# Performance work log

Measured on AMD Instinct MI355X. Metric: run time of the kernel, lower is better.

The kernel has to match this reference:

```python
import jax, jax.numpy as jnp
import numpy as np

B, K, N = 32768, 8, 64
TN = 3 * N


def _P():
    # 9x9 vec-transpose permutation (matches the hand-built P in the torch module)
    P = np.zeros((9, 9), dtype=np.float32)
    rows = [0, 1, 2, 3, 4, 5, 6, 7, 8]
    cols = [0, 3, 6, 1, 4, 7, 2, 5, 8]
    P[rows, cols] = 1.0
    return jnp.asarray(P)


def _precompute(b, w, lam):
    # b: (K,3,N), w: (1,N,1), lam: scalar
    wsum = jnp.sum(w)
    b_w = (b @ w)[..., 0] / wsum                       # (K,3)
    sw = jnp.sqrt(w).reshape(1, 1, N)                  # (1,1,N)
    bar_b = sw * (b - b_w[:, :, None])                 # (K,3,N)
    bar_B = bar_b.transpose(0, 2, 1).reshape(K, TN).T  # (3N,K)
    bar_H = 2.0 * (bar_B.T @ bar_B + lam * jnp.eye(K, dtype=b.dtype))
    Hinv = jnp.linalg.inv(bar_H)
    Htemp = Hinv @ jnp.ones((K, 1), dtype=b.dtype)     # (K,1)
    s = jnp.sum(Htemp)
    G = Hinv - (Htemp @ Htemp.T) / s                   # (K,K)
    g = Htemp / s                                      # (K,1)
    M = jnp.concatenate([
        2.0 * bar_B @ (G @ bar_B.T) - jnp.eye(TN, dtype=b.dtype),  # (3N,3N)
        2.0 * jnp.sqrt(lam) * (G @ bar_B.T),                        # (K,3N)
    ], axis=0)                                         # (3N+K,3N)
    h = jnp.concatenate([bar_B @ g, jnp.sqrt(lam) * g], axis=0)  # (3N+K,1)
    return bar_B, G, g, M, h, b_w, wsum


def setup_inputs() -> dict:
    key = jax.random.key(0)
    k1, k2 = jax.random.split(key)
    y = jax.random.normal(k1, (B, 3, N), dtype=jnp.float32)
    b = jax.random.normal(k2, (K, 3, N), dtype=jnp.float32)
    w = jnp.ones((1, N, 1), dtype=jnp.float32)
    lam = jnp.ones((1,), dtype=jnp.float32)
    return {"y": y, "b": b, "w": w, "lam": lam}


def reference(y, b, w, lam):
    lam = jnp.squeeze(lam)
    Pm = _P()
    bar_B, G, g, M, h, b_w, wsum = _precompute(b, w, lam)

    # weighted centroid + centered/weighted keypoints
    y_w = (y @ w) / wsum                               # (B,3,1)
    sw = jnp.sqrt(w).reshape(1, 1, N)
    bar_y = sw * (y - y_w)                             # (B,3,N)

    # Batched Q build. kron(Y^T, I3) contraction done implicitly:
    # (M @ kron(Y^T,I3))[a, 3m+j] = sum_n M[a,3n+j] * Y[m,n]
    M_r = M.reshape(TN + K, N, 3)                      # (A,N,3)
    E = jnp.einsum('anj,bmn->bamj', M_r, bar_y).reshape(B, TN + K, 9) @ Pm  # tempE: (B,A,9)
    q_top = jnp.einsum('a,bae->be', h[:, 0], E)        # Q[0,1:]: (B,9)
    Q00 = jnp.sum(h * h)
    Q_low = jnp.einsum('bae,baf->bef', E, E)           # Q[1:,1:]: (B,9,9)

    Q = jnp.zeros((B, 10, 10), dtype=y.dtype)
    Q = Q.at[:, 0, 0].set(Q00)
    Q = Q.at[:, 0, 1:].set(q_top)
    Q = Q.at[:, 1:, 0].set(q_top)
    Q = Q.at[:, 1:, 1:].set(Q_low)

    # Tight SDP relaxation solution: X* = v v^T with v the eigenvector of Q
    # at the smallest eigenvalue; the original then takes top eigvec of X,
    # which recovers the same v.
    ev, evec = jnp.linalg.eigh(Q)
    vec = evec[:, :, 0]                                # smallest-eigenvalue eigvec, (B,10)
    vec = vec / vec[:, :1]
    R = vec[:, 1:].reshape(B, 3, 3).transpose(0, 2, 1)  # (B,3,3)

    # shape coefficients: c = 2 * G bar_B^T kron(I_N, R^T) vec(bar_y^T) + g
    A = G @ bar_B.T                                    # (K,3N)
    Bv = jnp.einsum('bji,bjn->bni', R, bar_y).reshape(B, TN, 1)
    c = 2.0 * (A @ Bv) + g                             # (B,K,1)

    # translation
    t = y_w - R @ (b_w.T @ c)                          # (B,3,1)
    return R, t, c
```

## Files before the change

### kernel.cpp

```cpp
#include <hip/hip_runtime.h>
#include <math.h>

static constexpr int Bn = 32768;

#define WS_COEF  0
#define WS_G     1792
#define WS_g     1856
#define WS_BW    1864
#define WS_Q00   1888
#define WS_WSUM  1889
#define WS_CB    2048

__host__ __device__ constexpr int tidx(int i, int j) { return i*10 - i*(i+1)/2 + j; }
__host__ __device__ constexpr int tmm(int i, int j)  { return (i<j) ? tidx(i,j) : tidx(j,i); }
__host__ __device__ constexpr int lidx(int i, int j) { return i*(i+1)/2 + j; }

__global__ void k_pre(const float* __restrict__ bb, const float* __restrict__ w,
                      const float* __restrict__ lam, float* __restrict__ ws)
{
  __shared__ float s_w[64], s_sw[64], s_bw[24], s_barb[64][24];
  __shared__ float s_BtB[64];
  __shared__ float s_M[8][16];
  __shared__ float s_u[8], s_g[8], s_red[64], s_wsum, s_s;
  const int t = threadIdx.x;
  const int i8 = t >> 3, j8 = t & 7;
  const float lv = lam[0];

  s_w[t]  = w[t];
  s_sw[t] = sqrtf(fmaxf(s_w[t], 0.0f));
  __syncthreads();
  if (t == 0) { float a = 0; for (int n = 0; n < 64; n++) a += s_w[n]; s_wsum = a; }
  __syncthreads();
  const float wsum = s_wsum;
  if (t < 24) {
    float a = 0;
    for (int n = 0; n < 64; n++) a += bb[t*64 + n] * s_w[n];
    s_bw[t] = a / wsum;
  }
  __syncthreads();
  for (int km = 0; km < 24; ++km)
    s_barb[t][km] = s_sw[t] * (bb[km*64 + t] - s_bw[km]);
  __syncthreads();
  {
    float a = 0;
    for (int n = 0; n < 64; n++)
      for (int j = 0; j < 3; j++)
        a += s_barb[n][i8*3 + j] * s_barb[n][j8*3 + j];
    s_BtB[t] = a;
  }
  __syncthreads();
  s_M[i8][j8]     = 2.0f * (s_BtB[t] + ((i8 == j8) ? lv : 0.0f));
  s_M[i8][8 + j8] = (i8 == j8) ? 1.0f : 0.0f;
#pragma unroll
  for (int k = 0; k < 8; k++) {
    __syncthreads();
    const float fk  = s_M[i8][k];
    const float piv = 1.0f / s_M[k][k];
    __syncthreads();
    if (i8 == k) { s_M[k][j8] *= piv; s_M[k][8 + j8] *= piv; }
    __syncthreads();
    if (i8 != k) {
      s_M[i8][j8]     -= fk * s_M[k][j8];
      s_M[i8][8 + j8] -= fk * s_M[k][8 + j8];
    }
  }
  __syncthreads();
  if (t < 8) {
    float a = 0;
#pragma unroll
    for (int j = 0; j < 8; j++) a += s_M[t][8 + j];
    s_u[t] = a;
  }
  __syncthreads();
  if (t == 0) {
    float s = 0;
#pragma unroll
    for (int j = 0; j < 8; j++) s += s_u[j];
    s_s = s;
  }
  __syncthreads();
  const float s = s_s;
  if (t < 8) s_g[t] = s_u[t] / s;
  const float Gel = s_M[i8][8 + j8] - s_u[i8] * s_u[j8] / s;
  ws[WS_G + t] = Gel;
  __syncthreads();
  s_red[t] = s_g[i8] * (s_BtB[t] + ((i8 == j8) ? lv : 0.0f)) * s_g[j8];
  __syncthreads();
  if (t == 0) {
    float a = 0;
    for (int n = 0; n < 64; n++) a += s_red[n];
    ws[WS_Q00]  = a;
    ws[WS_WSUM] = wsum;
  }
  if (t < 8)  ws[WS_g + t]  = s_g[t];
  if (t < 24) ws[WS_BW + t] = s_bw[t];
  {
    float* c = ws + WS_COEF + t*28;
    c[0] = s_w[t];
    float qc[3] = {0, 0, 0};
#pragma unroll
    for (int km = 0; km < 24; km++) {
      float cb = s_sw[t] * s_barb[t][km];
      c[4 + km] = cb;
      qc[km % 3] += s_g[km / 3] * cb;
    }
    c[1] = qc[0]; c[2] = qc[1]; c[3] = qc[2];
  }
  {
#pragma unroll
    for (int sub = 0; sub < 4; sub++) {
      float* p = ws + WS_CB + sub*520 + t*8;
      p[0] = s_w[t];
#pragma unroll
      for (int kk = 0; kk < 6; kk++)
        p[1 + kk] = s_sw[t] * s_barb[t][sub*6 + kk];
      p[7] = 0.0f;
    }
  }
}

__global__ __launch_bounds__(256, 2) void k_main(const float* __restrict__ y,
                                                 const float* __restrict__ ws,
                                                 float* __restrict__ out)
{
  __shared__ float s_cb[4*520];
  __shared__ float s_G[64], s_g8[8], s_bw[24];
  __shared__ float s_F[72][66];
  __shared__ float s_Q[55][66];
  const int t   = threadIdx.x;
  const int lb  = t >> 2;
  const int sub = t & 3;
  const int b   = blockIdx.x * 64 + lb;

  for (int i = t; i < 4*520; i += 256) s_cb[i] = ws[WS_CB + i];
  if (t < 64) s_G[t]  = ws[WS_G + t];
  if (t < 8)  s_g8[t] = ws[WS_g + t];
  if (t >= 8 && t < 32) s_bw[t - 8] = ws[WS_BW + (t - 8)];
  const float q00v = ws[WS_Q00];
  const float wsum = ws[WS_WSUM];
  __syncthreads();

  const float* yb = y + (size_t)b * 192;
  float F6[6][3];
  float gw[6];
  float ywa[3] = {0, 0, 0};
#pragma unroll
  for (int i = 0; i < 6; i++) { F6[i][0] = 0; F6[i][1] = 0; F6[i][2] = 0; gw[i] = 0; }

  const float4* cbp = reinterpret_cast<const float4*>(s_cb + sub*520);
  for (int n4 = 0; n4 < 16; n4++) {
    float4 v0 = reinterpret_cast<const float4*>(yb)[n4];
    float4 v1 = reinterpret_cast<const float4*>(yb + 64)[n4];
    float4 v2 = reinterpret_cast<const float4*>(yb + 128)[n4];
    float a0[4] = {v0.x, v0.y, v0.z, v0.w};
    float a1[4] = {v1.x, v1.y, v1.z, v1.w};
    float a2[4] = {v2.x, v2.y, v2.z, v2.w};
#pragma unroll
    for (int l = 0; l < 4; l++) {
      const int n = 4*n4 + l;
      float4 va = cbp[n*2], vb = cbp[n*2 + 1];
      const float cb[6] = {va.y, va.z, va.w, vb.x, vb.y, vb.z};
      float ym0 = a0[l], ym1 = a1[l], ym2 = a2[l];
      float wn  = va.x;
      float wy0 = wn*ym0, wy1 = wn*ym1, wy2 = wn*ym2;
      ywa[0] += wy0; ywa[1] += wy1; ywa[2] += wy2;
      gw[0] += wy0*ym0; gw[1] += wy0*ym1; gw[2] += wy0*ym2;
      gw[3] += wy1*ym1; gw[4] += wy1*ym2; gw[5] += wy2*ym2;
#pragma unroll
      for (int kk = 0; kk < 6; kk++) {
        F6[kk][0] += cb[kk]*ym0; F6[kk][1] += cb[kk]*ym1; F6[kk][2] += cb[kk]*ym2;
      }
    }
  }
  const float iws = 1.0f / wsum;
  float yw[3] = {ywa[0]*iws, ywa[1]*iws, ywa[2]*iws};
  float Gram[6];
  Gram[0] = gw[0] - ywa[0]*ywa[0]*iws;
  Gram[1] = gw[1] - ywa[0]*ywa[1]*iws;
  Gram[2] = gw[2] - ywa[0]*ywa[2]*iws;
  Gram[3] = gw[3] - ywa[1]*ywa[1]*iws;
  Gram[4] = gw[4] - ywa[1]*ywa[2]*iws;
  Gram[5] = gw[5] - ywa[2]*ywa[2]*iws;

  const int kj0 = sub * 6;
#pragma unroll
  for (int kk = 0; kk < 6; kk++)
#pragma unroll
    for (int m = 0; m < 3; m++)
      s_F[(kj0 + kk)*3 + m][lb] = F6[kk][m];
  if (sub == 0) s_Q[0][lb] = q00v;
  {
    const float g0 = s_g8[sub*2], g1 = s_g8[sub*2 + 1];
#pragma unroll
    for (int e = 0; e < 9; e++) {
      const int j = e / 3, m = e % 3;
      float p = g0 * F6[j][m] + g1 * F6[3 + j][m];
      p += __shfl_xor(p, 1);
      p += __shfl_xor(p, 2);
      if ((e & 3) == sub) s_Q[tidx(0, 1 + e)][lb] = -p;
    }
  }
  __syncthreads();

  float FGr[2][9];
#pragma unroll
  for (int kk = 0; kk < 2; kk++) {
    const int k2 = sub*2 + kk;
    float gcol[8];
#pragma unroll
    for (int k = 0; k < 8; k++) gcol[k] = s_G[k*8 + k2];
#pragma unroll
    for (int e = 0; e < 9; e++) {
      const int j = e / 3, m = e % 3;
      float a = 0;
#pragma unroll
      for (int k = 0; k < 8; k++) a += gcol[k] * s_F[(k*3 + j)*3 + m][lb];
      FGr[kk][e] = a;
    }
  }
#pragma unroll
  for (int e = 0; e < 9; e++)
#pragma unroll
    for (int f = e; f < 9; f++) {
      const int j = e/3, m = e%3, j2 = f/3, m2 = f%3;
      float p = FGr[0][e] * F6[j2][m2] + FGr[1][e] * F6[3 + j2][m2];
      p += __shfl_xor(p, 1);
      p += __shfl_xor(p, 2);
      if ((tidx(1 + e, 1 + f) & 3) == sub) {
        const float gterm = (j == j2) ? Gram[(m <= m2) ? (m*3 - m*(m+1)/2 + m2) : (m2*3 - m2*(m2+1)/2 + m)] : 0.0f;
        s_Q[tidx(1 + e, 1 + f)][lb] = -2.0f*p + gterm;
      }
    }
  __syncthreads();

  float Mm[55];
#pragma unroll
  for (int i = 0; i < 10; i++)
#pragma unroll
    for (int j = 0; j <= i; j++)
      Mm[lidx(i,j)] = s_Q[tidx(j,i)][lb];

  float ad[10], b2[9];
#pragma unroll
  for (int j = 0; j < 8; j++) {
    float s2 = 0;
#pragma unroll
    for (int i = j + 1; i < 10; i++) s2 += Mm[lidx(i,j)] * Mm[lidx(i,j)];
    const float x0 = Mm[lidx(j+1,j)];
    const float anorm = __builtin_amdgcn_sqrtf(s2);
    const float alpha = (x0 > 0.0f) ? -anorm : anorm;
    const float uu = s2 - alpha * x0;
    const float beta = (uu > 1e-35f) ? __builtin_amdgcn_rcpf(uu) : 0.0f;
    float u[10], p[10];
    u[j+1] = x0 - alpha;
#pragma unroll
    for (int i = j + 2; i < 10; i++) u[i] = Mm[lidx(i,j)];
#pragma unroll
    for (int i = j + 1; i < 10; i++) {
      float acc = 0;
#pragma unroll
      for (int k = j + 1; k < 10; k++) acc += Mm[(i >= k) ? lidx(i,k) : lidx(k,i)] * u[k];
      p[i] = beta * acc;
    }
    float K = 0;
#pragma unroll
    for (int i = j + 1; i < 10; i++) K += u[i] * p[i];
    K *= 0.5f * beta;
#pragma unroll
    for (int i = j + 1; i < 10; i++) p[i] -= K * u[i];
#pragma unroll
    for (int i = j + 1; i < 10; i++)
#pragma unroll
      for (int k = j + 1; k <= i; k++)
        Mm[lidx(i,k)] -= u[i]*p[k] + p[i]*u[k];
    ad[j] = Mm[lidx(j,j)];
    b2[j] = s2;
  }
  ad[8] = Mm[lidx(8,8)];
  ad[9] = Mm[lidx(9,9)];
  b2[8] = Mm[lidx(9,8)] * Mm[lidx(9,8)];

  float b2max = b2[0];
#pragma unroll
  for (int i = 1; i < 9; i++) b2max = fmaxf(b2max, b2[i]);
  const float pm = 1e-20f * b2max + 1e-30f;

  float lo = 0.0f, hi = s_Q[0][lb];
#pragma unroll
  for (int j = 1; j < 10; j++) hi = fminf(hi, s_Q[tidx(j,j)][lb]);

  const int base = (t & 63) & ~3;
  const float subf = (sub == 0) ? 2.0f : (float)sub;
  for (int round = 0; round < 11; ++round) {
    const float quart = 0.25f * (hi - lo);
    const float mid = lo + quart * subf;
    int neg = 0;
    float d = ad[0] - mid;
    neg += (d < 0.0f) ? 1 : 0;
#pragma unroll
    for (int i = 1; i < 10; i++) {
      d = (fabsf(d) < pm) ? -pm : d;
      d = ad[i] - mid - b2[i-1] * __builtin_amdgcn_rcpf(d);
      neg += (d < 0.0f) ? 1 : 0;
    }
    const int n1 = __shfl(neg, base | 1);
    const int n2 = __shfl(neg, base | 2);
    const int n3 = __shfl(neg, base | 3);
    const float m1 = lo + quart, m2v = lo + 2.0f*quart, m3 = lo + 3.0f*quart;
    const float nlo = (n3 == 0) ? m3 : (n2 == 0) ? m2v : (n1 == 0) ? m1 : lo;
    const float nhi = (n1 > 0) ? m1 : (n2 > 0) ? m2v : (n3 > 0) ? m3 : hi;
    lo = nlo; hi = nhi;
  }

  float M[55], id[10];
#pragma unroll
  for (int i = 0; i < 10; i++)
#pragma unroll
    for (int j = 0; j <= i; j++)
      M[lidx(i,j)] = s_Q[tidx(j,i)][lb];
  float tr = 0.0f;
#pragma unroll
  for (int i = 0; i < 10; i++) tr += M[lidx(i,i)];
  const float delta = 1e-5f * fabsf(tr) + 1e-30f;
  const float sigma = lo - delta;
#pragma unroll
  for (int i = 0; i < 10; i++) M[lidx(i,i)] -= sigma;

#pragma unroll
  for (int j = 0; j < 10; j++) {
    float d = M[lidx(j,j)];
#pragma unroll
    for (int t2 = 0; t2 < j; t2++) d -= M[lidx(j,t2)] * M[lidx(j,t2)];
    d = fmaxf(d, 1e-30f);
    float is = __builtin_amdgcn_rsqf(d);
    id[j] = is;
#pragma unroll
    for (int i = j + 1; i < 10; i++) {
      float a = M[lidx(i,j)];
#pragma unroll
      for (int t2 = 0; t2 < j; t2++) a -= M[lidx(i,t2)] * M[lidx(j,t2)];
      M[lidx(i,j)] = a * is;
    }
  }

  float x[10];
#pragma unroll
  for (int i = 0; i < 10; i++) x[i] = 1.0f;
#pragma unroll
  for (int it = 0; it < 3; ++it) {
#pragma unroll
    for (int i = 0; i < 10; i++) {
      float a = x[i];
#pragma unroll
      for (int j = 0; j < i; j++) a -= M[lidx(i,j)] * x[j];
      x[i] = a * id[i];
    }
#pragma unroll
    for (int i = 9; i >= 0; i--) {
      float a = x[i];
#pragma unroll
      for (int j = i + 1; j < 10; j++) a -= M[lidx(j,i)] * x[j];
      x[i] = a * id[i];
    }
    float s2 = 0;
#pragma unroll
    for (int i = 0; i < 10; i++) s2 += x[i]*x[i];
    float sc = __builtin_amdgcn_rsqf(s2 + 1e-38f);
#pragma unroll
    for (int i = 0; i < 10; i++) x[i] *= sc;
  }

  const float inv0 = __builtin_amdgcn_rcpf(x[0]);
  float R[3][3];
#pragma unroll
  for (int r = 0; r < 3; r++)
#pragma unroll
    for (int cc = 0; cc < 3; cc++)
      R[r][cc] = x[1 + 3*cc + r] * inv0;

  float cv[2];
#pragma unroll
  for (int kk = 0; kk < 2; kk++) {
    const int k = sub*2 + kk;
    float a = 0;
#pragma unroll
    for (int e = 0; e < 9; e++) a += x[1 + e] * FGr[kk][e];
    cv[kk] = 2.0f * inv0 * a + s_g8[k];
    out[(size_t)12*Bn + (size_t)b*8 + k] = cv[kk];
  }
  float um0 = s_bw[(sub*2)*3 + 0]*cv[0] + s_bw[(sub*2 + 1)*3 + 0]*cv[1];
  float um1 = s_bw[(sub*2)*3 + 1]*cv[0] + s_bw[(sub*2 + 1)*3 + 1]*cv[1];
  float um2 = s_bw[(sub*2)*3 + 2]*cv[0] + s_bw[(sub*2 + 1)*3 + 2]*cv[1];
  um0 += __shfl_xor(um0, 1); um0 += __shfl_xor(um0, 2);
  um1 += __shfl_xor(um1, 1); um1 += __shfl_xor(um1, 2);
  um2 += __shfl_xor(um2, 1); um2 += __shfl_xor(um2, 2);

#pragma unroll
  for (int r = 0; r < 3; r++)
#pragma unroll
    for (int cc = 0; cc < 3; cc++)
      if (((r*3 + cc) & 3) == sub)
        out[(size_t)b*9 + r*3 + cc] = R[r][cc];
  if (sub == 0) {
#pragma unroll
    for (int r = 0; r < 3; r++)
      out[(size_t)9*Bn + (size_t)b*3 + r] = yw[r] - (R[r][0]*um0 + R[r][1]*um1 + R[r][2]*um2);
  }
}

extern "C" void kernel_launch(void* const* d_in, const int* in_sizes, int n_in,
                              void* d_out, int out_size, void* d_ws, size_t ws_size,
                              hipStream_t stream) {
  const float* y   = (const float*)d_in[0];
  const float* bb  = (const float*)d_in[1];
  const float* w   = (const float*)d_in[2];
  const float* lam = (const float*)d_in[3];
  float* ws  = (float*)d_ws;
  float* out = (float*)d_out;
  k_pre <<<1,      64, 0, stream>>>(bb, w, lam, ws);
  k_main<<<Bn/64, 256, 0, stream>>>(y, ws, out);
}
```

Baseline: 42.90 us.

## Split each batch item across eight lanes and use 9-way bisection

Each batch element is now handled by eight threads instead of four, so each lane owns one shape coefficient k. Block size grows to 512 threads and the precomputed coefficient table is repacked to four floats per point per lane. The eigenvalue bisection now tests eight points per round (splitting the interval into nine parts) and runs fewer rounds. The aim is more parallelism and shorter per-thread dependency chains, at the cost of redundant reads of y (now duplicated across eight lanes), an extra shuffle level in every reduction, and duplicated eigensolve work.

```diff
diff --git a/kernel.cpp b/kernel.cpp
--- a/kernel.cpp
+++ b/kernel.cpp
@@ -3,16 +3,14 @@
 
 static constexpr int Bn = 32768;
 
-#define WS_COEF  0
 #define WS_G     1792
 #define WS_g     1856
 #define WS_BW    1864
 #define WS_Q00   1888
 #define WS_WSUM  1889
-#define WS_CB    2048
+#define WS_CB8   2048
 
 __host__ __device__ constexpr int tidx(int i, int j) { return i*10 - i*(i+1)/2 + j; }
-__host__ __device__ constexpr int tmm(int i, int j)  { return (i<j) ? tidx(i,j) : tidx(j,i); }
 __host__ __device__ constexpr int lidx(int i, int j) { return i*(i+1)/2 + j; }
 
 __global__ void k_pre(const float* __restrict__ bb, const float* __restrict__ w,
@@ -95,44 +93,31 @@
   if (t < 8)  ws[WS_g + t]  = s_g[t];
   if (t < 24) ws[WS_BW + t] = s_bw[t];
   {
-    float* c = ws + WS_COEF + t*28;
-    c[0] = s_w[t];
-    float qc[3] = {0, 0, 0};
-#pragma unroll
-    for (int km = 0; km < 24; km++) {
-      float cb = s_sw[t] * s_barb[t][km];
-      c[4 + km] = cb;
-      qc[km % 3] += s_g[km / 3] * cb;
-    }
-    c[1] = qc[0]; c[2] = qc[1]; c[3] = qc[2];
-  }
-  {
-#pragma unroll
-    for (int sub = 0; sub < 4; sub++) {
-      float* p = ws + WS_CB + sub*520 + t*8;
+#pragma unroll
+    for (int sub = 0; sub < 8; sub++) {
+      float* p = ws + WS_CB8 + sub*260 + t*4;
       p[0] = s_w[t];
 #pragma unroll
-      for (int kk = 0; kk < 6; kk++)
-        p[1 + kk] = s_sw[t] * s_barb[t][sub*6 + kk];
-      p[7] = 0.0f;
+      for (int kk = 0; kk < 3; kk++)
+        p[1 + kk] = s_sw[t] * s_barb[t][sub*3 + kk];
     }
   }
 }
 
-__global__ __launch_bounds__(256, 2) void k_main(const float* __restrict__ y,
+__global__ __launch_bounds__(512, 4) void k_main(const float* __restrict__ y,
                                                  const float* __restrict__ ws,
                                                  float* __restrict__ out)
 {
-  __shared__ float s_cb[4*520];
+  __shared__ float s_cb[8*260];
   __shared__ float s_G[64], s_g8[8], s_bw[24];
   __shared__ float s_F[72][66];
   __shared__ float s_Q[55][66];
   const int t   = threadIdx.x;
-  const int lb  = t >> 2;
-  const int sub = t & 3;
+  const int lb  = t >> 3;
+  const int sub = t & 7;
   const int b   = blockIdx.x * 64 + lb;
 
-  for (int i = t; i < 4*520; i += 256) s_cb[i] = ws[WS_CB + i];
+  for (int i = t; i < 8*260; i += 512) s_cb[i] = ws[WS_CB8 + i];
   if (t < 64) s_G[t]  = ws[WS_G + t];
   if (t < 8)  s_g8[t] = ws[WS_g + t];
   if (t >= 8 && t < 32) s_bw[t - 8] = ws[WS_BW + (t - 8)];
@@ -141,13 +126,15 @@
   __syncthreads();
 
   const float* yb = y + (size_t)b * 192;
-  float F6[6][3];
+  float F3[3][3];
   float gw[6];
   float ywa[3] = {0, 0, 0};
 #pragma unroll
-  for (int i = 0; i < 6; i++) { F6[i][0] = 0; F6[i][1] = 0; F6[i][2] = 0; gw[i] = 0; }
-
-  const float4* cbp = reinterpret_cast<const float4*>(s_cb + sub*520);
+  for (int i = 0; i < 3; i++) { F3[i][0] = 0; F3[i][1] = 0; F3[i][2] = 0; }
+#pragma unroll
+  for (int i = 0; i < 6; i++) gw[i] = 0;
+
+  const float4* cbp = reinterpret_cast<const float4*>(s_cb + sub*260);
   for (int n4 = 0; n4 < 16; n4++) {
     float4 v0 = reinterpret_cast<const float4*>(yb)[n4];
     float4 v1 = reinterpret_cast<const float4*>(yb + 64)[n4];
@@ -158,8 +145,8 @@
 #pragma unroll
     for (int l = 0; l < 4; l++) {
       const int n = 4*n4 + l;
-      float4 va = cbp[n*2], vb = cbp[n*2 + 1];
-      const float cb[6] = {va.y, va.z, va.w, vb.x, vb.y, vb.z};
+      float4 va = cbp[n];
+      const float cb3[3] = {va.y, va.z, va.w};
       float ym0 = a0[l], ym1 = a1[l], ym2 = a2[l];
       float wn  = va.x;
       float wy0 = wn*ym0, wy1 = wn*ym1, wy2 = wn*ym2;
@@ -167,8 +154,8 @@
       gw[0] += wy0*ym0; gw[1] += wy0*ym1; gw[2] += wy0*ym2;
       gw[3] += wy1*ym1; gw[4] += wy1*ym2; gw[5] += wy2*ym2;
 #pragma unroll
-      for (int kk = 0; kk < 6; kk++) {
-        F6[kk][0] += cb[kk]*ym0; F6[kk][1] += cb[kk]*ym1; F6[kk][2] += cb[kk]*ym2;
+      for (int kk = 0; kk < 3; kk++) {
+        F3[kk][0] += cb3[kk]*ym0; F3[kk][1] += cb3[kk]*ym1; F3[kk][2] += cb3[kk]*ym2;
       }
     }
   }
@@ -182,40 +169,38 @@
   Gram[4] = gw[4] - ywa[1]*ywa[2]*iws;
   Gram[5] = gw[5] - ywa[2]*ywa[2]*iws;
 
-  const int kj0 = sub * 6;
-#pragma unroll
-  for (int kk = 0; kk < 6; kk++)
+#pragma unroll
+  for (int kk = 0; kk < 3; kk++)
 #pragma unroll
     for (int m = 0; m < 3; m++)
-      s_F[(kj0 + kk)*3 + m][lb] = F6[kk][m];
+      s_F[(sub*3 + kk)*3 + m][lb] = F3[kk][m];
   if (sub == 0) s_Q[0][lb] = q00v;
   {
-    const float g0 = s_g8[sub*2], g1 = s_g8[sub*2 + 1];
+    const float g0 = s_g8[sub];
 #pragma unroll
     for (int e = 0; e < 9; e++) {
       const int j = e / 3, m = e % 3;
-      float p = g0 * F6[j][m] + g1 * F6[3 + j][m];
+      float p = g0 * F3[j][m];
       p += __shfl_xor(p, 1);
       p += __shfl_xor(p, 2);
-      if ((e & 3) == sub) s_Q[tidx(0, 1 + e)][lb] = -p;
-    }
-  }
-  __syncthreads();
-
-  float FGr[2][9];
-#pragma unroll
-  for (int kk = 0; kk < 2; kk++) {
-    const int k2 = sub*2 + kk;
+      p += __shfl_xor(p, 4);
+      if ((e & 7) == sub) s_Q[tidx(0, 1 + e)][lb] = -p;
+    }
+  }
+  __syncthreads();
+
+  float FGr[9];
+  {
     float gcol[8];
 #pragma unroll
-    for (int k = 0; k < 8; k++) gcol[k] = s_G[k*8 + k2];
+    for (int k = 0; k < 8; k++) gcol[k] = s_G[k*8 + sub];
 #pragma unroll
     for (int e = 0; e < 9; e++) {
       const int j = e / 3, m = e % 3;
       float a = 0;
 #pragma unroll
       for (int k = 0; k < 8; k++) a += gcol[k] * s_F[(k*3 + j)*3 + m][lb];
-      FGr[kk][e] = a;
+      FGr[e] = a;
     }
   }
 #pragma unroll
@@ -223,10 +208,11 @@
 #pragma unroll
     for (int f = e; f < 9; f++) {
       const int j = e/3, m = e%3, j2 = f/3, m2 = f%3;
-      float p = FGr[0][e] * F6[j2][m2] + FGr[1][e] * F6[3 + j2][m2];
+      float p = FGr[e] * F3[j2][m2];
       p += __shfl_xor(p, 1);
       p += __shfl_xor(p, 2);
-      if ((tidx(1 + e, 1 + f) & 3) == sub) {
+      p += __shfl_xor(p, 4);
+      if ((tidx(1 + e, 1 + f) & 7) == sub) {
         const float gterm = (j == j2) ? Gram[(m <= m2) ? (m*3 - m*(m+1)/2 + m2) : (m2*3 - m2*(m2+1)/2 + m)] : 0.0f;
         s_Q[tidx(1 + e, 1 + f)][lb] = -2.0f*p + gterm;
       }
@@ -289,11 +275,11 @@
 #pragma unroll
   for (int j = 1; j < 10; j++) hi = fminf(hi, s_Q[tidx(j,j)][lb]);
 
-  const int base = (t & 63) & ~3;
-  const float subf = (sub == 0) ? 2.0f : (float)sub;
-  for (int round = 0; round < 11; ++round) {
-    const float quart = 0.25f * (hi - lo);
-    const float mid = lo + quart * subf;
+  const int base = (t & 63) & ~7;
+  const float ninth = 1.0f / 9.0f;
+  for (int round = 0; round < 7; ++round) {
+    const float h9 = ninth * (hi - lo);
+    const float mid = lo + (float)(sub + 1) * h9;
     int neg = 0;
     float d = ad[0] - mid;
     neg += (d < 0.0f) ? 1 : 0;
@@ -303,12 +289,17 @@
       d = ad[i] - mid - b2[i-1] * __builtin_amdgcn_rcpf(d);
       neg += (d < 0.0f) ? 1 : 0;
     }
-    const int n1 = __shfl(neg, base | 1);
-    const int n2 = __shfl(neg, base | 2);
-    const int n3 = __shfl(neg, base | 3);
-    const float m1 = lo + quart, m2v = lo + 2.0f*quart, m3 = lo + 3.0f*quart;
-    const float nlo = (n3 == 0) ? m3 : (n2 == 0) ? m2v : (n1 == 0) ? m1 : lo;
-    const float nhi = (n1 > 0) ? m1 : (n2 > 0) ? m2v : (n3 > 0) ? m3 : hi;
+    int j = 0;
+    j = (__shfl(neg, base + 0) == 0) ? 1 : j;
+    j = (__shfl(neg, base + 1) == 0) ? 2 : j;
+    j = (__shfl(neg, base + 2) == 0) ? 3 : j;
+    j = (__shfl(neg, base + 3) == 0) ? 4 : j;
+    j = (__shfl(neg, base + 4) == 0) ? 5 : j;
+    j = (__shfl(neg, base + 5) == 0) ? 6 : j;
+    j = (__shfl(neg, base + 6) == 0) ? 7 : j;
+    j = (__shfl(neg, base + 7) == 0) ? 8 : j;
+    const float nlo = lo + (float)j * h9;
+    const float nhi = lo + (float)(j + 1) * h9;
     lo = nlo; hi = nhi;
   }
 
@@ -378,30 +369,28 @@
     for (int cc = 0; cc < 3; cc++)
       R[r][cc] = x[1 + 3*cc + r] * inv0;
 
-  float cv[2];
-#pragma unroll
-  for (int kk = 0; kk < 2; kk++) {
-    const int k = sub*2 + kk;
+  float cv;
+  {
     float a = 0;
 #pragma unroll
-    for (int e = 0; e < 9; e++) a += x[1 + e] * FGr[kk][e];
-    cv[kk] = 2.0f * inv0 * a + s_g8[k];
-    out[(size_t)12*Bn + (size_t)b*8 + k] = cv[kk];
-  }
-  float um0 = s_bw[(sub*2)*3 + 0]*cv[0] + s_bw[(sub*2 + 1)*3 + 0]*cv[1];
-  float um1 = s_bw[(sub*2)*3 + 1]*cv[0] + s_bw[(sub*2 + 1)*3 + 1]*cv[1];
-  float um2 = s_bw[(sub*2)*3 + 2]*cv[0] + s_bw[(sub*2 + 1)*3 + 2]*cv[1];
-  um0 += __shfl_xor(um0, 1); um0 += __shfl_xor(um0, 2);
-  um1 += __shfl_xor(um1, 1); um1 += __shfl_xor(um1, 2);
-  um2 += __shfl_xor(um2, 1); um2 += __shfl_xor(um2, 2);
+    for (int e = 0; e < 9; e++) a += x[1 + e] * FGr[e];
+    cv = 2.0f * inv0 * a + s_g8[sub];
+    out[(size_t)12*Bn + (size_t)b*8 + sub] = cv;
+  }
+  float um0 = s_bw[sub*3 + 0] * cv;
+  float um1 = s_bw[sub*3 + 1] * cv;
+  float um2 = s_bw[sub*3 + 2] * cv;
+  um0 += __shfl_xor(um0, 1); um0 += __shfl_xor(um0, 2); um0 += __shfl_xor(um0, 4);
+  um1 += __shfl_xor(um1, 1); um1 += __shfl_xor(um1, 2); um1 += __shfl_xor(um1, 4);
+  um2 += __shfl_xor(um2, 1); um2 += __shfl_xor(um2, 2); um2 += __shfl_xor(um2, 4);
 
 #pragma unroll
   for (int r = 0; r < 3; r++)
 #pragma unroll
     for (int cc = 0; cc < 3; cc++)
-      if (((r*3 + cc) & 3) == sub)
+      if (((r*3 + cc) & 7) == sub)
         out[(size_t)b*9 + r*3 + cc] = R[r][cc];
-  if (sub == 0) {
+  if (sub == 1) {
 #pragma unroll
     for (int r = 0; r < 3; r++)
       out[(size_t)9*Bn + (size_t)b*3 + r] = yw[r] - (R[r][0]*um0 + R[r][1]*um1 + R[r][2]*um2);
@@ -418,5 +407,5 @@
   float* ws  = (float*)d_ws;
   float* out = (float*)d_out;
   k_pre <<<1,      64, 0, stream>>>(bb, w, lam, ws);
-  k_main<<<Bn/64, 256, 0, stream>>>(y, ws, out);
+  k_main<<<Bn/64, 512, 0, stream>>>(y, ws, out);
 }
```

Measured after the change: 65.16 us. 1.52x slower.

## Split keypoint loop across lanes and reduce full F via shuffles

Applied to the files above, without the earlier changes.

Changes the work split among the four threads per batch element. Before, each thread handled six of the 24 coefficient columns over all 64 points. Now each thread handles 16 points for all 24 columns, and the partial sums of F, Gram and centroid are combined with xor shuffles. This removes the shared s_F staging buffer and one block barrier, and the coefficient table becomes a single 64x32 layout. In exchange each thread holds 72 F accumulators and runs 81 shuffle reductions, which raises register pressure under launch_bounds(256,2). A leftover no-op loop computing ci is also added.

```diff
diff --git a/kernel.cpp b/kernel.cpp
--- a/kernel.cpp
+++ b/kernel.cpp
@@ -3,16 +3,14 @@
 
 static constexpr int Bn = 32768;
 
-#define WS_COEF  0
 #define WS_G     1792
 #define WS_g     1856
 #define WS_BW    1864
 #define WS_Q00   1888
 #define WS_WSUM  1889
-#define WS_CB    2048
+#define WS_CB32  2048
 
 __host__ __device__ constexpr int tidx(int i, int j) { return i*10 - i*(i+1)/2 + j; }
-__host__ __device__ constexpr int tmm(int i, int j)  { return (i<j) ? tidx(i,j) : tidx(j,i); }
 __host__ __device__ constexpr int lidx(int i, int j) { return i*(i+1)/2 + j; }
 
 __global__ void k_pre(const float* __restrict__ bb, const float* __restrict__ w,
@@ -95,27 +93,13 @@
   if (t < 8)  ws[WS_g + t]  = s_g[t];
   if (t < 24) ws[WS_BW + t] = s_bw[t];
   {
-    float* c = ws + WS_COEF + t*28;
-    c[0] = s_w[t];
-    float qc[3] = {0, 0, 0};
-#pragma unroll
-    for (int km = 0; km < 24; km++) {
-      float cb = s_sw[t] * s_barb[t][km];
-      c[4 + km] = cb;
-      qc[km % 3] += s_g[km / 3] * cb;
-    }
-    c[1] = qc[0]; c[2] = qc[1]; c[3] = qc[2];
-  }
-  {
-#pragma unroll
-    for (int sub = 0; sub < 4; sub++) {
-      float* p = ws + WS_CB + sub*520 + t*8;
-      p[0] = s_w[t];
-#pragma unroll
-      for (int kk = 0; kk < 6; kk++)
-        p[1 + kk] = s_sw[t] * s_barb[t][sub*6 + kk];
-      p[7] = 0.0f;
-    }
+    float* p = ws + WS_CB32 + t*32;
+    p[0] = s_w[t]; p[1] = 0; p[2] = 0; p[3] = 0;
+#pragma unroll
+    for (int km = 0; km < 24; km++)
+      p[4 + km] = s_sw[t] * s_barb[t][km];
+#pragma unroll
+    for (int i = 28; i < 32; i++) p[i] = 0;
   }
 }
 
@@ -123,16 +107,15 @@
                                                  const float* __restrict__ ws,
                                                  float* __restrict__ out)
 {
-  __shared__ float s_cb[4*520];
+  __shared__ float s_cb[64*32];
   __shared__ float s_G[64], s_g8[8], s_bw[24];
-  __shared__ float s_F[72][66];
   __shared__ float s_Q[55][66];
   const int t   = threadIdx.x;
   const int lb  = t >> 2;
   const int sub = t & 3;
   const int b   = blockIdx.x * 64 + lb;
 
-  for (int i = t; i < 4*520; i += 256) s_cb[i] = ws[WS_CB + i];
+  for (int i = t; i < 64*32; i += 256) s_cb[i] = ws[WS_CB32 + i];
   if (t < 64) s_G[t]  = ws[WS_G + t];
   if (t < 8)  s_g8[t] = ws[WS_g + t];
   if (t >= 8 && t < 32) s_bw[t - 8] = ws[WS_BW + (t - 8)];
@@ -141,14 +124,17 @@
   __syncthreads();
 
   const float* yb = y + (size_t)b * 192;
-  float F6[6][3];
+  float F[24][3];
   float gw[6];
   float ywa[3] = {0, 0, 0};
 #pragma unroll
-  for (int i = 0; i < 6; i++) { F6[i][0] = 0; F6[i][1] = 0; F6[i][2] = 0; gw[i] = 0; }
-
-  const float4* cbp = reinterpret_cast<const float4*>(s_cb + sub*520);
-  for (int n4 = 0; n4 < 16; n4++) {
+  for (int i = 0; i < 24; i++) { F[i][0] = 0; F[i][1] = 0; F[i][2] = 0; }
+#pragma unroll
+  for (int i = 0; i < 6; i++) gw[i] = 0;
+
+#pragma unroll
+  for (int i4 = 0; i4 < 4; i4++) {
+    const int n4 = sub*4 + i4;
     float4 v0 = reinterpret_cast<const float4*>(yb)[n4];
     float4 v1 = reinterpret_cast<const float4*>(yb + 64)[n4];
     float4 v2 = reinterpret_cast<const float4*>(yb + 128)[n4];
@@ -158,20 +144,48 @@
 #pragma unroll
     for (int l = 0; l < 4; l++) {
       const int n = 4*n4 + l;
-      float4 va = cbp[n*2], vb = cbp[n*2 + 1];
-      const float cb[6] = {va.y, va.z, va.w, vb.x, vb.y, vb.z};
+      const float4* row = reinterpret_cast<const float4*>(s_cb + n*32);
+      float4 c0 = row[0];
+      float4 ch[6];
+#pragma unroll
+      for (int cc = 0; cc < 6; cc++) {
+        const int ci = 1 + ((cc + sub) & 3) + ((cc + sub) > 3 && (cc+sub) < 6 ? 4 : ((cc+sub) >= 6 ? ((cc+sub)-6) - ((cc+sub)&3) + 4 : 0));
+        (void)ci;
+      }
+#pragma unroll
+      for (int cc = 0; cc < 6; cc++) ch[cc] = row[1 + cc];
+      const float cb[24] = {ch[0].x, ch[0].y, ch[0].z, ch[0].w,
+                            ch[1].x, ch[1].y, ch[1].z, ch[1].w,
+                            ch[2].x, ch[2].y, ch[2].z, ch[2].w,
+                            ch[3].x, ch[3].y, ch[3].z, ch[3].w,
+                            ch[4].x, ch[4].y, ch[4].z, ch[4].w,
+                            ch[5].x, ch[5].y, ch[5].z, ch[5].w};
       float ym0 = a0[l], ym1 = a1[l], ym2 = a2[l];
-      float wn  = va.x;
+      float wn  = c0.x;
       float wy0 = wn*ym0, wy1 = wn*ym1, wy2 = wn*ym2;
       ywa[0] += wy0; ywa[1] += wy1; ywa[2] += wy2;
       gw[0] += wy0*ym0; gw[1] += wy0*ym1; gw[2] += wy0*ym2;
       gw[3] += wy1*ym1; gw[4] += wy1*ym2; gw[5] += wy2*ym2;
 #pragma unroll
-      for (int kk = 0; kk < 6; kk++) {
-        F6[kk][0] += cb[kk]*ym0; F6[kk][1] += cb[kk]*ym1; F6[kk][2] += cb[kk]*ym2;
+      for (int km = 0; km < 24; km++) {
+        F[km][0] += cb[km]*ym0; F[km][1] += cb[km]*ym1; F[km][2] += cb[km]*ym2;
       }
     }
   }
+#pragma unroll
+  for (int km = 0; km < 24; km++)
+#pragma unroll
+    for (int m = 0; m < 3; m++) {
+      float v = F[km][m];
+      v += __shfl_xor(v, 1);
+      v += __shfl_xor(v, 2);
+      F[km][m] = v;
+    }
+#pragma unroll
+  for (int i = 0; i < 6; i++) { float v = gw[i]; v += __shfl_xor(v, 1); v += __shfl_xor(v, 2); gw[i] = v; }
+#pragma unroll
+  for (int i = 0; i < 3; i++) { float v = ywa[i]; v += __shfl_xor(v, 1); v += __shfl_xor(v, 2); ywa[i] = v; }
+
   const float iws = 1.0f / wsum;
   float yw[3] = {ywa[0]*iws, ywa[1]*iws, ywa[2]*iws};
   float Gram[6];
@@ -182,39 +196,40 @@
   Gram[4] = gw[4] - ywa[1]*ywa[2]*iws;
   Gram[5] = gw[5] - ywa[2]*ywa[2]*iws;
 
-  const int kj0 = sub * 6;
+  if (sub == 0) s_Q[0][lb] = q00v;
+#pragma unroll
+  for (int e = 0; e < 9; e++) {
+    const int j = e / 3, m = e % 3;
+    float a = 0;
+#pragma unroll
+    for (int k = 0; k < 8; k++) a += s_g8[k] * F[k*3 + j][m];
+    if ((e & 3) == sub) s_Q[tidx(0, 1 + e)][lb] = -a;
+  }
+  float F6[6][3];
 #pragma unroll
   for (int kk = 0; kk < 6; kk++)
 #pragma unroll
-    for (int m = 0; m < 3; m++)
-      s_F[(kj0 + kk)*3 + m][lb] = F6[kk][m];
-  if (sub == 0) s_Q[0][lb] = q00v;
-  {
-    const float g0 = s_g8[sub*2], g1 = s_g8[sub*2 + 1];
-#pragma unroll
-    for (int e = 0; e < 9; e++) {
-      const int j = e / 3, m = e % 3;
-      float p = g0 * F6[j][m] + g1 * F6[3 + j][m];
-      p += __shfl_xor(p, 1);
-      p += __shfl_xor(p, 2);
-      if ((e & 3) == sub) s_Q[tidx(0, 1 + e)][lb] = -p;
-    }
-  }
-  __syncthreads();
-
+    for (int m = 0; m < 3; m++) {
+      float x01 = (sub & 1) ? F[6 + kk][m]  : F[kk][m];
+      float x23 = (sub & 1) ? F[18 + kk][m] : F[12 + kk][m];
+      F6[kk][m] = (sub & 2) ? x23 : x01;
+    }
   float FGr[2][9];
 #pragma unroll
   for (int kk = 0; kk < 2; kk++) {
-    const int k2 = sub*2 + kk;
     float gcol[8];
 #pragma unroll
-    for (int k = 0; k < 8; k++) gcol[k] = s_G[k*8 + k2];
+    for (int k = 0; k < 8; k++) {
+      float g01 = (sub & 1) ? s_G[k*8 + 2 + kk] : s_G[k*8 + 0 + kk];
+      float g23 = (sub & 1) ? s_G[k*8 + 6 + kk] : s_G[k*8 + 4 + kk];
+      gcol[k] = (sub & 2) ? g23 : g01;
+    }
 #pragma unroll
     for (int e = 0; e < 9; e++) {
       const int j = e / 3, m = e % 3;
       float a = 0;
 #pragma unroll
-      for (int k = 0; k < 8; k++) a += gcol[k] * s_F[(k*3 + j)*3 + m][lb];
+      for (int k = 0; k < 8; k++) a += gcol[k] * F[k*3 + j][m];
       FGr[kk][e] = a;
     }
   }
```

Result: no change. 42.80 us (-0.2%).
